# Performance work log

Hardware: AMD Instinct MI355X
Metric: run time of the kernel (lower is better)

The kernel has to match this reference:

```python
import jax, jax.numpy as jnp
import numpy as np

B, S, D = 2, 2048, 1024
H = 16
DK = D // H  # 64

def setup_inputs() -> dict:
    key = jax.random.key(0)
    ks = jax.random.split(key, 7)
    scale = 1.0 / np.sqrt(D)
    return {
        "Query": jax.random.normal(ks[0], (B, S, D), dtype=jnp.float32),
        "Key":   jax.random.normal(ks[1], (B, S, D), dtype=jnp.float32),
        "Value": jax.random.normal(ks[2], (B, S, D), dtype=jnp.float32),
        "Wq": jax.random.normal(ks[3], (D, D), dtype=jnp.float32) * scale,
        "Wk": jax.random.normal(ks[4], (D, D), dtype=jnp.float32) * scale,
        "Wv": jax.random.normal(ks[5], (D, D), dtype=jnp.float32) * scale,
        "Wo": jax.random.normal(ks[6], (D, D), dtype=jnp.float32) * scale,
    }

def reference(Query, Key, Value, Wq, Wk, Wv, Wo):
    b = Query.shape[0]
    # nn.Linear(bias=False): x @ W.T ; reshape to [B, H, S, DK]
    q = (Query @ Wq.T).reshape(b, -1, H, DK).transpose(0, 2, 1, 3)
    k = (Key   @ Wk.T).reshape(b, -1, H, DK).transpose(0, 2, 1, 3)
    v = (Value @ Wv.T).reshape(b, -1, H, DK).transpose(0, 2, 1, 3)
    # full O(S^2) score matrix [B, H, Sq, Sk]
    scores = jnp.einsum("bhqd,bhkd->bhqk", q, k) / jnp.sqrt(jnp.float32(DK))
    # FAITHFUL to source: nn.Softmax(dim=1) normalizes over the HEAD axis
    attn = jax.nn.softmax(scores, axis=1)
    ctx = jnp.einsum("bhqk,bhkd->bhqd", attn, v)  # [B, H, Sq, DK]
    ctx = ctx.transpose(0, 2, 1, 3).reshape(b, -1, H * DK)  # [B, S, D]
    return ctx @ Wo.T
```

## Files before the change

kernel.cpp:

```cpp
#include <hip/hip_runtime.h>
#include <stdint.h>

#define BB   2
#define SS   2048
#define DD   1024
#define HH   16
#define DKK  64
#define MM   (BB*SS)

typedef __attribute__((ext_vector_type(4))) float f32x4;
typedef __attribute__((ext_vector_type(8))) short s16x8;

#define MFMA_B16(a, b, c) __builtin_amdgcn_mfma_f32_16x16x32_bf16((a), (b), (c), 0, 0, 0)

__device__ __forceinline__ ushort f2bf(float f) {
  uint u = __float_as_uint(f);
  u += 0x7FFFu + ((u >> 16) & 1u);
  return (ushort)(u >> 16);
}
__device__ __forceinline__ float bf2f(ushort u) {
  return __uint_as_float((uint)u << 16);
}
__device__ __forceinline__ s16x8 cvt8(const float* src) {
  float4 a = *(const float4*)src, b = *(const float4*)(src + 4);
  union { ushort u[8]; s16x8 v; } r;
  r.u[0] = f2bf(a.x); r.u[1] = f2bf(a.y); r.u[2] = f2bf(a.z); r.u[3] = f2bf(a.w);
  r.u[4] = f2bf(b.x); r.u[5] = f2bf(b.y); r.u[6] = f2bf(b.z); r.u[7] = f2bf(b.w);
  return r.v;
}

__global__ void cvt_kernel(const float* __restrict__ src, ushort* __restrict__ dst, int n) {
  int i = (blockIdx.x * 256 + threadIdx.x) * 8;
  if (i >= n) return;
  *(s16x8*)(dst + i) = cvt8(src + i);
}

__global__ __launch_bounds__(256, 2) void qkv_proj(
    const float* __restrict__ Ia, const float* __restrict__ Ib, const float* __restrict__ Ic,
    const ushort* __restrict__ Wa, const ushort* __restrict__ Wb, const ushort* __restrict__ Wc,
    ushort* __restrict__ Oa, ushort* __restrict__ Ob, ushort* __restrict__ Oc)
{
  __shared__ ushort As[128 * 32];
  __shared__ ushort Bs[128 * 32];
  const int tid  = threadIdx.x;
  const int lane = tid & 63, wave = tid >> 6;
  const int q = lane & 15, g = lane >> 4;
  const int wr = wave >> 1, wc = wave & 1;
  const int mblk = blockIdx.x * 128, nblk = blockIdx.y * 128;
  const int mode = blockIdx.z;

  const float*  A = (mode == 0) ? Ia : (mode == 1) ? Ib : Ic;
  const ushort* W = (mode == 0) ? Wa : (mode == 1) ? Wb : Wc;

  f32x4 acc[4][4];
  {
    f32x4 z = {0.f, 0.f, 0.f, 0.f};
#pragma unroll
    for (int i = 0; i < 4; ++i)
#pragma unroll
      for (int j = 0; j < 4; ++j) acc[i][j] = z;
  }

  const int r0 = tid >> 2;
  const int e0 = (tid & 3) * 8;
  for (int k0 = 0; k0 < 1024; k0 += 32) {
#pragma unroll
    for (int it = 0; it < 2; ++it) {
      const int row = r0 + it * 64;
      *(s16x8*)&As[row * 32 + e0] = cvt8(A + (size_t)(mblk + row) * 1024 + k0 + e0);
      *(s16x8*)&Bs[row * 32 + e0] = *(const s16x8*)(W + (size_t)(nblk + row) * 1024 + k0 + e0);
    }
    __syncthreads();
    s16x8 af[4], bf[4];
#pragma unroll
    for (int t = 0; t < 4; ++t) {
      af[t] = *(const s16x8*)&As[(wr * 64 + t * 16 + q) * 32 + g * 8];
      bf[t] = *(const s16x8*)&Bs[(wc * 64 + t * 16 + q) * 32 + g * 8];
    }
#pragma unroll
    for (int mt = 0; mt < 4; ++mt)
#pragma unroll
      for (int nt = 0; nt < 4; ++nt)
        acc[mt][nt] = MFMA_B16(af[mt], bf[nt], acc[mt][nt]);
    __syncthreads();
  }

  if (mode == 2) {
    ushort* Vt = Oc;
#pragma unroll
    for (int mt = 0; mt < 4; ++mt)
#pragma unroll
      for (int nt = 0; nt < 4; ++nt) {
        const int s0 = mblk + wr * 64 + mt * 16 + g * 4;
        const int o  = nblk + wc * 64 + nt * 16 + q;
        const int h = o >> 6, dk = o & 63;
        const int b = s0 >> 11, sr = s0 & 2047;
        ushort4 pk;
        pk.x = f2bf(acc[mt][nt][0]); pk.y = f2bf(acc[mt][nt][1]);
        pk.z = f2bf(acc[mt][nt][2]); pk.w = f2bf(acc[mt][nt][3]);
        *(ushort4*)(Vt + ((size_t)((b * 16 + h) * 64 + dk)) * SS + sr) = pk;
      }
  } else {
    const float scale = (mode == 0) ? 0.125f : 1.0f;
    ushort* P = (mode == 0) ? Oa : Ob;
    ushort* wl = As + wave * 1024;
    const int h0 = (nblk + wc * 64) >> 6;
#pragma unroll
    for (int mt = 0; mt < 4; ++mt) {
      const int s0 = mblk + wr * 64 + mt * 16;
      const int b  = s0 >> 11, sr0 = s0 & 2047;
#pragma unroll
      for (int nt = 0; nt < 4; ++nt)
#pragma unroll
        for (int j = 0; j < 4; ++j)
          wl[(g * 4 + j) * 64 + nt * 16 + q] = f2bf(acc[mt][nt][j] * scale);
#pragma unroll
      for (int it = 0; it < 2; ++it) {
        s16x8 v = *(const s16x8*)((char*)wl + it * 1024 + lane * 16);
        const int lr = it * 8 + (lane >> 3);
        const int c  = (lane & 7) * 8;
        *(s16x8*)(P + ((size_t)((b * 16 + h0) * SS) + sr0 + lr) * DKK + c) = v;
      }
    }
  }
}

__global__ __launch_bounds__(256, 2) void o_proj(
    const ushort* __restrict__ A, const ushort* __restrict__ W,
    float* __restrict__ O)
{
  __shared__ ushort As[128 * 32];
  __shared__ ushort Bs[128 * 32];
  const int tid  = threadIdx.x;
  const int lane = tid & 63, wave = tid >> 6;
  const int q = lane & 15, g = lane >> 4;
  const int wr = wave >> 1, wc = wave & 1;
  const int mblk = blockIdx.x * 128, nblk = blockIdx.y * 128;

  f32x4 acc[4][4];
  {
    f32x4 z = {0.f, 0.f, 0.f, 0.f};
#pragma unroll
    for (int i = 0; i < 4; ++i)
#pragma unroll
      for (int j = 0; j < 4; ++j) acc[i][j] = z;
  }

  const int r0 = tid >> 2;
  const int e0 = (tid & 3) * 8;
  for (int k0 = 0; k0 < 1024; k0 += 32) {
#pragma unroll
    for (int it = 0; it < 2; ++it) {
      const int row = r0 + it * 64;
      *(s16x8*)&As[row * 32 + e0] = *(const s16x8*)(A + (size_t)(mblk + row) * 1024 + k0 + e0);
      *(s16x8*)&Bs[row * 32 + e0] = *(const s16x8*)(W + (size_t)(nblk + row) * 1024 + k0 + e0);
    }
    __syncthreads();
    s16x8 af[4], bf[4];
#pragma unroll
    for (int t = 0; t < 4; ++t) {
      af[t] = *(const s16x8*)&As[(wr * 64 + t * 16 + q) * 32 + g * 8];
      bf[t] = *(const s16x8*)&Bs[(wc * 64 + t * 16 + q) * 32 + g * 8];
    }
#pragma unroll
    for (int mt = 0; mt < 4; ++mt)
#pragma unroll
      for (int nt = 0; nt < 4; ++nt)
        acc[mt][nt] = MFMA_B16(af[mt], bf[nt], acc[mt][nt]);
    __syncthreads();
  }

#pragma unroll
  for (int mt = 0; mt < 4; ++mt)
#pragma unroll
    for (int nt = 0; nt < 4; ++nt)
#pragma unroll
      for (int j = 0; j < 4; ++j) {
        const int s = mblk + wr * 64 + mt * 16 + g * 4 + j;
        const int o = nblk + wc * 64 + nt * 16 + q;
        O[(size_t)s * DD + o] = acc[mt][nt][j];
      }
}

__global__ __launch_bounds__(256, 2) void den_kernel(
    const ushort* __restrict__ Qp, const ushort* __restrict__ Kp,
    ushort* __restrict__ Rden)
{
  __shared__ ushort smem[2][8192];
  const int tid  = threadIdx.x;
  const int lane = tid & 63, wave = tid >> 6;
  const int q = lane & 15, g = lane >> 4;
  const int wr = wave >> 1, wc = wave & 1;
  const int kblk = blockIdx.x * 128, qblk = blockIdx.y * 128;
  const int b = blockIdx.z;

  f32x4 den[4][4], acc[4][4];
  {
    f32x4 z = {0.f, 0.f, 0.f, 0.f};
#pragma unroll
    for (int i = 0; i < 4; ++i)
#pragma unroll
      for (int j = 0; j < 4; ++j) { den[i][j] = z; acc[i][j] = z; }
  }

  const int r0 = tid >> 2;
  const int e0 = (tid & 3) * 8;

  {
    const ushort* Kh = Kp + ((size_t)(b * 16) * SS + kblk) * DKK;
    const ushort* Qh = Qp + ((size_t)(b * 16) * SS + qblk) * DKK;
    *(s16x8*)&smem[0][r0 * 32 + e0]        = *(const s16x8*)(Kh + (size_t)r0 * DKK + e0);
    *(s16x8*)&smem[0][(r0 + 64) * 32 + e0] = *(const s16x8*)(Kh + (size_t)(r0 + 64) * DKK + e0);
    *(s16x8*)&smem[0][4096 + r0 * 32 + e0]        = *(const s16x8*)(Qh + (size_t)r0 * DKK + e0);
    *(s16x8*)&smem[0][4096 + (r0 + 64) * 32 + e0] = *(const s16x8*)(Qh + (size_t)(r0 + 64) * DKK + e0);
  }
  __syncthreads();

  for (int s = 0; s < 32; ++s) {
    const int cur = s & 1;
    s16x8 nA0, nA1, nB0, nB1;
    if (s < 31) {
      const int h1 = (s + 1) >> 1, d1 = ((s + 1) & 1) * 32;
      const ushort* Kh = Kp + ((size_t)(b * 16 + h1) * SS + kblk) * DKK + d1;
      const ushort* Qh = Qp + ((size_t)(b * 16 + h1) * SS + qblk) * DKK + d1;
      nA0 = *(const s16x8*)(Kh + (size_t)r0 * DKK + e0);
      nA1 = *(const s16x8*)(Kh + (size_t)(r0 + 64) * DKK + e0);
      nB0 = *(const s16x8*)(Qh + (size_t)r0 * DKK + e0);
      nB1 = *(const s16x8*)(Qh + (size_t)(r0 + 64) * DKK + e0);
    }
    s16x8 af[4], bf[4];
#pragma unroll
    for (int t = 0; t < 4; ++t) {
      af[t] = *(const s16x8*)&smem[cur][(wr * 64 + t * 16 + q) * 32 + g * 8];
      bf[t] = *(const s16x8*)&smem[cur][4096 + (wc * 64 + t * 16 + q) * 32 + g * 8];
    }
#pragma unroll
    for (int mt = 0; mt < 4; ++mt)
#pragma unroll
      for (int nt = 0; nt < 4; ++nt)
        acc[mt][nt] = MFMA_B16(af[mt], bf[nt], acc[mt][nt]);
    if (s & 1) {
      f32x4 z = {0.f, 0.f, 0.f, 0.f};
#pragma unroll
      for (int mt = 0; mt < 4; ++mt)
#pragma unroll
        for (int nt = 0; nt < 4; ++nt) {
#pragma unroll
          for (int r = 0; r < 4; ++r)
            den[mt][nt][r] += __expf(acc[mt][nt][r]);
          acc[mt][nt] = z;
        }
    }
    if (s < 31) {
      *(s16x8*)&smem[cur ^ 1][r0 * 32 + e0]        = nA0;
      *(s16x8*)&smem[cur ^ 1][(r0 + 64) * 32 + e0] = nA1;
      *(s16x8*)&smem[cur ^ 1][4096 + r0 * 32 + e0]        = nB0;
      *(s16x8*)&smem[cur ^ 1][4096 + (r0 + 64) * 32 + e0] = nB1;
    }
    __syncthreads();
  }

  char* aw2 = (char*)smem + wave * 8192;
#pragma unroll
  for (int mt = 0; mt < 4; ++mt)
#pragma unroll
    for (int nt = 0; nt < 4; ++nt) {
      const int ql = nt * 16 + q;
      ushort4 pk;
      pk.x = f2bf(1.0f / den[mt][nt][0]);
      pk.y = f2bf(1.0f / den[mt][nt][1]);
      pk.z = f2bf(1.0f / den[mt][nt][2]);
      pk.w = f2bf(1.0f / den[mt][nt][3]);
      *(ushort4*)(aw2 + ql * 128 + ((mt * 32 + g * 8) ^ ((ql & 7) << 4))) = pk;
    }
#pragma unroll
  for (int it = 0; it < 8; ++it) {
    const int idx = it * 64 + lane;
    const int row = idx >> 3;
    const int seg = idx & 7;
    s16x8 v = *(const s16x8*)(aw2 + row * 128 + ((seg * 16) ^ ((row & 7) << 4)));
    *(s16x8*)(Rden + (size_t)b * SS * SS
              + (size_t)(qblk + wc * 64 + row) * SS
              + kblk + wr * 64 + seg * 8) = v;
  }
}

__global__ __launch_bounds__(512, 2) void attn5_kernel(
    const ushort* __restrict__ Qp, const ushort* __restrict__ Kp,
    const ushort* __restrict__ Vt, const ushort* __restrict__ Rden,
    ushort* __restrict__ Ctx)
{
  __shared__ ushort Ktile[2][64 * 64];
  __shared__ ushort Vtile[2][64 * 64];
  __shared__ ushort Rw_all[8][16 * 64];
  __shared__ ushort aw_all[8][16 * 64];

  const int tid  = threadIdx.x;
  const int lane = tid & 63;
  const int w    = tid >> 6;
  const int q    = lane & 15;
  const int g    = lane >> 4;
  const int bid  = blockIdx.x;
  const int bh   = bid & 31;
  const int b    = bh >> 4, h = bh & 15;
  const int qblk = (bid >> 5) * 128;

  const ushort* Qb = Qp + ((size_t)bh * SS + qblk + w * 16 + q) * DKK + g * 8;
  s16x8 qf0 = *(const s16x8*)(Qb);
  s16x8 qf1 = *(const s16x8*)(Qb + 32);

  const ushort* Ks = Kp + (size_t)bh * SS * DKK;
  const ushort* Vs = Vt + (size_t)bh * DKK * SS;
  const ushort* Rs = Rden + (size_t)b * SS * SS + (size_t)(qblk + w * 16) * SS;

  f32x4 acc[4];
  {
    f32x4 z = {0.f, 0.f, 0.f, 0.f};
#pragma unroll
    for (int n = 0; n < 4; ++n) acc[n] = z;
  }

  ushort* Rw = Rw_all[w];
  ushort* aw = aw_all[w];
  const int srow = tid >> 3, sseg = tid & 7;
  const int sd   = (sseg * 8) ^ ((srow & 7) << 3);
  const int r16  = lane >> 2;
  const int sgA  = (lane & 3) * 2;
  const int rd0  = r16 * 64 + ((sgA * 8) ^ ((r16 & 7) << 3));
  const int rd1  = r16 * 64 + (((sgA + 1) * 8) ^ ((r16 & 7) << 3));

  {
    s16x8 gK  = *(const s16x8*)(Ks + tid * 8);
    s16x8 gV  = *(const s16x8*)(Vs + (size_t)srow * SS + sseg * 8);
    s16x8 gR0 = *(const s16x8*)(Rs + (size_t)r16 * SS + sgA * 8);
    s16x8 gR1 = *(const s16x8*)(Rs + (size_t)r16 * SS + (sgA + 1) * 8);
    *(s16x8*)&Ktile[0][srow * 64 + sd] = gK;
    *(s16x8*)&Vtile[0][srow * 64 + sd] = gV;
    *(s16x8*)&Rw[rd0] = gR0;
    *(s16x8*)&Rw[rd1] = gR1;
  }
  __syncthreads();

  for (int kt = 0; kt < 32; ++kt) {
    const int cur = kt & 1;
    s16x8 gK, gV, gR0, gR1;
    if (kt < 31) {
      const int k1 = (kt + 1) * 64;
      gK  = *(const s16x8*)(Ks + (size_t)k1 * DKK + tid * 8);
      gV  = *(const s16x8*)(Vs + (size_t)srow * SS + k1 + sseg * 8);
      gR0 = *(const s16x8*)(Rs + (size_t)r16 * SS + k1 + sgA * 8);
      gR1 = *(const s16x8*)(Rs + (size_t)r16 * SS + k1 + (sgA + 1) * 8);
    }
    const ushort* Kt = Ktile[cur];
    const ushort* Vv = Vtile[cur];

#pragma unroll
    for (int ks = 0; ks < 4; ++ks) {
      const int kr = ks * 16 + q;
      s16x8 a0 = *(const s16x8*)&Kt[kr * 64 + ((g * 8) ^ ((kr & 7) << 3))];
      s16x8 a1 = *(const s16x8*)&Kt[kr * 64 + ((32 + g * 8) ^ ((kr & 7) << 3))];
      f32x4 c = {0.f, 0.f, 0.f, 0.f};
      c = MFMA_B16(a0, qf0, c);
      c = MFMA_B16(a1, qf1, c);
      ushort4 rv = *(const ushort4*)&Rw[q * 64 + (((ks * 2 + (g >> 1)) ^ (q & 7)) * 8) + (g & 1) * 4];
      float p0 = __expf(c[0]) * bf2f(rv.x);
      float p1 = __expf(c[1]) * bf2f(rv.y);
      float p2 = __expf(c[2]) * bf2f(rv.z);
      float p3 = __expf(c[3]) * bf2f(rv.w);
      uint2 pp;
      asm("v_cvt_pk_bf16_f32 %0, %1, %2" : "=v"(pp.x) : "v"(p0), "v"(p1));
      asm("v_cvt_pk_bf16_f32 %0, %1, %2" : "=v"(pp.y) : "v"(p2), "v"(p3));
      *(uint2*)&aw[q * 64 + ((ks * 16 + g * 4) ^ ((q & 7) << 3))] = pp;
    }
#pragma unroll
    for (int kc = 0; kc < 2; ++kc) {
      s16x8 vf[4];
#pragma unroll
      for (int n = 0; n < 4; ++n) {
        const int vr = n * 16 + q;
        vf[n] = *(const s16x8*)&Vv[vr * 64 + ((kc * 32 + g * 8) ^ ((vr & 7) << 3))];
      }
      s16x8 pa = *(const s16x8*)&aw[q * 64 + ((kc * 32 + g * 8) ^ ((q & 7) << 3))];
#pragma unroll
      for (int n = 0; n < 4; ++n)
        acc[n] = MFMA_B16(pa, vf[n], acc[n]);
    }
    if (kt < 31) {
      *(s16x8*)&Ktile[cur ^ 1][srow * 64 + sd] = gK;
      *(s16x8*)&Vtile[cur ^ 1][srow * 64 + sd] = gV;
      *(s16x8*)&Rw[rd0] = gR0;
      *(s16x8*)&Rw[rd1] = gR1;
    }
    __syncthreads();
  }

#pragma unroll
  for (int n = 0; n < 4; ++n)
#pragma unroll
    for (int j = 0; j < 4; ++j)
      aw[(g * 4 + j) * 64 + n * 16 + q] = f2bf(acc[n][j]);
  ushort* P = Ctx + ((size_t)(b * SS) + qblk + w * 16) * DD + h * 64;
#pragma unroll
  for (int it = 0; it < 2; ++it) {
    const int idx = it * 64 + lane;
    const int row = idx >> 3;
    const int seg = idx & 7;
    s16x8 v = *(const s16x8*)&aw[row * 64 + seg * 8];
    *(s16x8*)(P + (size_t)row * DD + seg * 8) = v;
  }
}

extern "C" void kernel_launch(void* const* d_in, const int* in_sizes, int n_in,
                              void* d_out, int out_size, void* d_ws, size_t ws_size,
                              hipStream_t stream) {
  const float* Query = (const float*)d_in[0];
  const float* Key   = (const float*)d_in[1];
  const float* Value = (const float*)d_in[2];
  const float* Wq    = (const float*)d_in[3];
  const float* Wk    = (const float*)d_in[4];
  const float* Wv    = (const float*)d_in[5];
  const float* Wo    = (const float*)d_in[6];

  size_t off = 0;
  char* ws = (char*)d_ws;
  auto alloc = [&](size_t bytes) -> void* {
    void* p = ws + off;
    off += (bytes + 255) & ~(size_t)255;
    return p;
  };
  const size_t nX = (size_t)MM * DD;
  const size_t nW = (size_t)DD * DD;
  const size_t nS = (size_t)BB * SS * SS;
  ushort* Wqb  = (ushort*)alloc(nW * 2);
  ushort* Wkb  = (ushort*)alloc(nW * 2);
  ushort* Wvb  = (ushort*)alloc(nW * 2);
  ushort* Wob  = (ushort*)alloc(nW * 2);
  ushort* Qp   = (ushort*)alloc(nX * 2);
  ushort* Kp   = (ushort*)alloc(nX * 2);
  ushort* Vtb  = (ushort*)alloc(nX * 2);
  ushort* Rden = (ushort*)alloc(nS * 2);
  ushort* Ctx  = (ushort*)alloc(nX * 2);

  cvt_kernel<<<(int)(nW / 2048), 256, 0, stream>>>(Wq, Wqb, (int)nW);
  cvt_kernel<<<(int)(nW / 2048), 256, 0, stream>>>(Wk, Wkb, (int)nW);
  cvt_kernel<<<(int)(nW / 2048), 256, 0, stream>>>(Wv, Wvb, (int)nW);
  cvt_kernel<<<(int)(nW / 2048), 256, 0, stream>>>(Wo, Wob, (int)nW);

  qkv_proj<<<dim3(32, 8, 3), 256, 0, stream>>>(
      Query, Key, Value, Wqb, Wkb, Wvb, Qp, Kp, Vtb);

  den_kernel<<<dim3(16, 16, 2), 256, 0, stream>>>(Qp, Kp, Rden);
  attn5_kernel<<<512, 512, 0, stream>>>(Qp, Kp, Vtb, Rden, Ctx);

  o_proj<<<dim3(32, 8), 256, 0, stream>>>(Ctx, Wob, (float*)d_out);
}
```

Measured before the change: 177.3 us.

## Stage full-head K/Q tiles in den kernel and fold log2e into Q scale

The denominator kernel now loads a whole 64-wide head per pipeline stage into a swizzled, doubled shared buffer. This halves the loop trip count and syncs, and keeps the score accumulator local to each head. Log2(e) is folded into the Q projection scale so both den and attention kernels use exp2 directly instead of __expf. Float-to-bf16 conversions in cvt8 and the reciprocal store use packed hardware conversion instructions. The larger shared footprint (64KB per block) may reduce occupancy.

```diff
diff --git a/kernel.cpp b/kernel.cpp
--- a/kernel.cpp
+++ b/kernel.cpp
@@ -21,13 +21,19 @@
 __device__ __forceinline__ float bf2f(ushort u) {
   return __uint_as_float((uint)u << 16);
 }
+#define EXP2(x) exp2f(x)
+
 __device__ __forceinline__ s16x8 cvt8(const float* src) {
   float4 a = *(const float4*)src, b = *(const float4*)(src + 4);
-  union { ushort u[8]; s16x8 v; } r;
-  r.u[0] = f2bf(a.x); r.u[1] = f2bf(a.y); r.u[2] = f2bf(a.z); r.u[3] = f2bf(a.w);
-  r.u[4] = f2bf(b.x); r.u[5] = f2bf(b.y); r.u[6] = f2bf(b.z); r.u[7] = f2bf(b.w);
+  union { uint u[4]; s16x8 v; } r;
+  asm("v_cvt_pk_bf16_f32 %0, %1, %2" : "=v"(r.u[0]) : "v"(a.x), "v"(a.y));
+  asm("v_cvt_pk_bf16_f32 %0, %1, %2" : "=v"(r.u[1]) : "v"(a.z), "v"(a.w));
+  asm("v_cvt_pk_bf16_f32 %0, %1, %2" : "=v"(r.u[2]) : "v"(b.x), "v"(b.y));
+  asm("v_cvt_pk_bf16_f32 %0, %1, %2" : "=v"(r.u[3]) : "v"(b.z), "v"(b.w));
   return r.v;
 }
+
+#define QSCALE (0.125f * 1.4426950408889634f)
 
 __global__ void cvt_kernel(const float* __restrict__ src, ushort* __restrict__ dst, int n) {
   int i = (blockIdx.x * 256 + threadIdx.x) * 8;
@@ -101,7 +107,7 @@
         *(ushort4*)(Vt + ((size_t)((b * 16 + h) * 64 + dk)) * SS + sr) = pk;
       }
   } else {
-    const float scale = (mode == 0) ? 0.125f : 1.0f;
+    const float scale = (mode == 0) ? QSCALE : 1.0f;
     ushort* P = (mode == 0) ? Oa : Ob;
     ushort* wl = As + wave * 1024;
     const int h0 = (nblk + wc * 64) >> 6;
@@ -186,7 +192,7 @@
     const ushort* __restrict__ Qp, const ushort* __restrict__ Kp,
     ushort* __restrict__ Rden)
 {
-  __shared__ ushort smem[2][8192];
+  __shared__ ushort smem[2][16384];
   const int tid  = threadIdx.x;
   const int lane = tid & 63, wave = tid >> 6;
   const int q = lane & 15, g = lane >> 4;
@@ -194,68 +200,70 @@
   const int kblk = blockIdx.x * 128, qblk = blockIdx.y * 128;
   const int b = blockIdx.z;
 
-  f32x4 den[4][4], acc[4][4];
+  f32x4 den[4][4];
   {
     f32x4 z = {0.f, 0.f, 0.f, 0.f};
 #pragma unroll
     for (int i = 0; i < 4; ++i)
 #pragma unroll
-      for (int j = 0; j < 4; ++j) { den[i][j] = z; acc[i][j] = z; }
-  }
-
-  const int r0 = tid >> 2;
-  const int e0 = (tid & 3) * 8;
-
-  {
-    const ushort* Kh = Kp + ((size_t)(b * 16) * SS + kblk) * DKK;
-    const ushort* Qh = Qp + ((size_t)(b * 16) * SS + qblk) * DKK;
-    *(s16x8*)&smem[0][r0 * 32 + e0]        = *(const s16x8*)(Kh + (size_t)r0 * DKK + e0);
-    *(s16x8*)&smem[0][(r0 + 64) * 32 + e0] = *(const s16x8*)(Kh + (size_t)(r0 + 64) * DKK + e0);
-    *(s16x8*)&smem[0][4096 + r0 * 32 + e0]        = *(const s16x8*)(Qh + (size_t)r0 * DKK + e0);
-    *(s16x8*)&smem[0][4096 + (r0 + 64) * 32 + e0] = *(const s16x8*)(Qh + (size_t)(r0 + 64) * DKK + e0);
+      for (int j = 0; j < 4; ++j) den[i][j] = z;
+  }
+
+  const int srow = tid >> 3, sseg = tid & 7;
+  const int sd   = (sseg * 8) ^ ((srow & 7) << 3);
+
+  const ushort* Kb0 = Kp + ((size_t)(b * 16) * SS + kblk) * DKK;
+  const ushort* Qb0 = Qp + ((size_t)(b * 16) * SS + qblk) * DKK;
+
+#pragma unroll
+  for (int i = 0; i < 4; ++i) {
+    const int row = srow + i * 32;
+    *(s16x8*)&smem[0][row * 64 + sd]        = *(const s16x8*)(Kb0 + (size_t)row * DKK + sseg * 8);
+    *(s16x8*)&smem[0][8192 + row * 64 + sd] = *(const s16x8*)(Qb0 + (size_t)row * DKK + sseg * 8);
   }
   __syncthreads();
 
-  for (int s = 0; s < 32; ++s) {
+  for (int s = 0; s < 16; ++s) {
     const int cur = s & 1;
-    s16x8 nA0, nA1, nB0, nB1;
-    if (s < 31) {
-      const int h1 = (s + 1) >> 1, d1 = ((s + 1) & 1) * 32;
-      const ushort* Kh = Kp + ((size_t)(b * 16 + h1) * SS + kblk) * DKK + d1;
-      const ushort* Qh = Qp + ((size_t)(b * 16 + h1) * SS + qblk) * DKK + d1;
-      nA0 = *(const s16x8*)(Kh + (size_t)r0 * DKK + e0);
-      nA1 = *(const s16x8*)(Kh + (size_t)(r0 + 64) * DKK + e0);
-      nB0 = *(const s16x8*)(Qh + (size_t)r0 * DKK + e0);
-      nB1 = *(const s16x8*)(Qh + (size_t)(r0 + 64) * DKK + e0);
-    }
-    s16x8 af[4], bf[4];
+    s16x8 nA[4], nB[4];
+    if (s < 15) {
+      const ushort* Kh = Kb0 + (size_t)(s + 1) * SS * DKK;
+      const ushort* Qh = Qb0 + (size_t)(s + 1) * SS * DKK;
+#pragma unroll
+      for (int i = 0; i < 4; ++i) {
+        const int row = srow + i * 32;
+        nA[i] = *(const s16x8*)(Kh + (size_t)row * DKK + sseg * 8);
+        nB[i] = *(const s16x8*)(Qh + (size_t)row * DKK + sseg * 8);
+      }
+    }
+    s16x8 af[4][2], bf[4][2];
 #pragma unroll
     for (int t = 0; t < 4; ++t) {
-      af[t] = *(const s16x8*)&smem[cur][(wr * 64 + t * 16 + q) * 32 + g * 8];
-      bf[t] = *(const s16x8*)&smem[cur][4096 + (wc * 64 + t * 16 + q) * 32 + g * 8];
+      const int ra = wr * 64 + t * 16 + q;
+      const int rb = wc * 64 + t * 16 + q;
+      af[t][0] = *(const s16x8*)&smem[cur][ra * 64 + ((g * 8) ^ ((ra & 7) << 3))];
+      af[t][1] = *(const s16x8*)&smem[cur][ra * 64 + ((32 + g * 8) ^ ((ra & 7) << 3))];
+      bf[t][0] = *(const s16x8*)&smem[cur][8192 + rb * 64 + ((g * 8) ^ ((rb & 7) << 3))];
+      bf[t][1] = *(const s16x8*)&smem[cur][8192 + rb * 64 + ((32 + g * 8) ^ ((rb & 7) << 3))];
     }
 #pragma unroll
     for (int mt = 0; mt < 4; ++mt)
 #pragma unroll
-      for (int nt = 0; nt < 4; ++nt)
-        acc[mt][nt] = MFMA_B16(af[mt], bf[nt], acc[mt][nt]);
-    if (s & 1) {
-      f32x4 z = {0.f, 0.f, 0.f, 0.f};
-#pragma unroll
-      for (int mt = 0; mt < 4; ++mt)
-#pragma unroll
-        for (int nt = 0; nt < 4; ++nt) {
-#pragma unroll
-          for (int r = 0; r < 4; ++r)
-            den[mt][nt][r] += __expf(acc[mt][nt][r]);
-          acc[mt][nt] = z;
-        }
-    }
-    if (s < 31) {
-      *(s16x8*)&smem[cur ^ 1][r0 * 32 + e0]        = nA0;
-      *(s16x8*)&smem[cur ^ 1][(r0 + 64) * 32 + e0] = nA1;
-      *(s16x8*)&smem[cur ^ 1][4096 + r0 * 32 + e0]        = nB0;
-      *(s16x8*)&smem[cur ^ 1][4096 + (r0 + 64) * 32 + e0] = nB1;
+      for (int nt = 0; nt < 4; ++nt) {
+        f32x4 c = {0.f, 0.f, 0.f, 0.f};
+        c = MFMA_B16(af[mt][0], bf[nt][0], c);
+        c = MFMA_B16(af[mt][1], bf[nt][1], c);
+#pragma unroll
+        for (int r = 0; r < 4; ++r)
+          den[mt][nt][r] += EXP2(c[r]);
+      }
+    if (s < 15) {
+#pragma unroll
+      for (int i = 0; i < 4; ++i) {
+        const int row = srow + i * 32;
+        *(s16x8*)&smem[cur ^ 1][row * 64 + sd]        = nA[i];
+        *(s16x8*)&smem[cur ^ 1][8192 + row * 64 + sd] = nB[i];
+      }
     }
     __syncthreads();
   }
@@ -266,12 +274,12 @@
 #pragma unroll
     for (int nt = 0; nt < 4; ++nt) {
       const int ql = nt * 16 + q;
-      ushort4 pk;
-      pk.x = f2bf(1.0f / den[mt][nt][0]);
-      pk.y = f2bf(1.0f / den[mt][nt][1]);
-      pk.z = f2bf(1.0f / den[mt][nt][2]);
-      pk.w = f2bf(1.0f / den[mt][nt][3]);
-      *(ushort4*)(aw2 + ql * 128 + ((mt * 32 + g * 8) ^ ((ql & 7) << 4))) = pk;
+      const float i0 = 1.0f / den[mt][nt][0], i1 = 1.0f / den[mt][nt][1];
+      const float i2 = 1.0f / den[mt][nt][2], i3 = 1.0f / den[mt][nt][3];
+      uint2 pk;
+      asm("v_cvt_pk_bf16_f32 %0, %1, %2" : "=v"(pk.x) : "v"(i0), "v"(i1));
+      asm("v_cvt_pk_bf16_f32 %0, %1, %2" : "=v"(pk.y) : "v"(i2), "v"(i3));
+      *(uint2*)(aw2 + ql * 128 + ((mt * 32 + g * 8) ^ ((ql & 7) << 4))) = pk;
     }
 #pragma unroll
   for (int it = 0; it < 8; ++it) {
@@ -363,10 +371,10 @@
       c = MFMA_B16(a0, qf0, c);
       c = MFMA_B16(a1, qf1, c);
       ushort4 rv = *(const ushort4*)&Rw[q * 64 + (((ks * 2 + (g >> 1)) ^ (q & 7)) * 8) + (g & 1) * 4];
-      float p0 = __expf(c[0]) * bf2f(rv.x);
-      float p1 = __expf(c[1]) * bf2f(rv.y);
-      float p2 = __expf(c[2]) * bf2f(rv.z);
-      float p3 = __expf(c[3]) * bf2f(rv.w);
+      float p0 = EXP2(c[0]) * bf2f(rv.x);
+      float p1 = EXP2(c[1]) * bf2f(rv.y);
+      float p2 = EXP2(c[2]) * bf2f(rv.z);
+      float p3 = EXP2(c[3]) * bf2f(rv.w);
       uint2 pp;
       asm("v_cvt_pk_bf16_f32 %0, %1, %2" : "=v"(pp.x) : "v"(p0), "v"(p1));
       asm("v_cvt_pk_bf16_f32 %0, %1, %2" : "=v"(pp.y) : "v"(p2), "v"(p3));
```

New measurement: 190.0 us. 1.07x slower.
